# Kernel tuning notes

Measured on AMD Instinct MI355X. Metric: run time of the kernel, lower is better.

The kernel has to match this reference:

```python
import jax, jax.numpy as jnp
import numpy as np

N_NODES = 100000
N_EDGES = 500000
STALK_DIM = 16
N_TYPES = 8


def setup_inputs() -> dict:
    key = jax.random.key(0)
    k1, k2, k3, k4, k5 = jax.random.split(key, 5)
    entity_reps = jax.random.normal(k1, (STALK_DIM, N_NODES), dtype=jnp.float32)
    restriction_maps = jax.random.normal(k2, (N_TYPES, N_TYPES, STALK_DIM, STALK_DIM), dtype=jnp.float32) / STALK_DIM
    src = jax.random.randint(k3, (N_EDGES,), 0, N_NODES, dtype=jnp.int64) if jax.config.jax_enable_x64 else jax.random.randint(k3, (N_EDGES,), 0, N_NODES, dtype=jnp.int32)
    dst = jax.random.randint(k4, (N_EDGES,), 0, N_NODES, dtype=src.dtype)
    edge_index = jnp.stack([src, dst], axis=0)  # [2, E]
    entity_types = jax.random.randint(k5, (N_NODES,), 0, N_TYPES, dtype=src.dtype)
    return {"entity_reps": entity_reps, "restriction_maps": restriction_maps,
            "edge_index": edge_index, "entity_types": entity_types}


def reference(entity_reps, restriction_maps, edge_index, entity_types):
    d, n_nodes = entity_reps.shape
    n_edges = edge_index.shape[1]
    src, dst = edge_index[0], edge_index[1]

    # _get_degs: in-degree (over col) ^ -1/2, inf -> 0
    deg = jax.ops.segment_sum(jnp.ones((n_edges,), entity_reps.dtype), dst,
                              num_segments=n_nodes)
    inv_node_degs = jnp.where(deg > 0, deg ** -0.5, jnp.zeros_like(deg))

    # entity_reps @ diag(inv_node_degs): scale each node column
    x = entity_reps * inv_node_degs[None, :]  # [d, N]

    et_src = entity_types[src]  # [E]
    et_dst = entity_types[dst]  # [E]

    # Gather per-edge restriction maps [E,d,d], then replicate the original's
    # raw memory reshape to (d, d, E) (a reinterpretation, NOT a transpose).
    head_maps = restriction_maps[et_src, et_dst].reshape(d, d, n_edges)
    tail_maps = restriction_maps[et_dst, et_src].reshape(d, d, n_edges)

    # Batched per-edge matvec: head_embeddings[:, e] = head_maps[:, :, e] @ x[:, src[e]]
    head_emb = jnp.einsum('ije,je->ie', head_maps, x[:, src])  # [d, E]
    tail_emb = jnp.einsum('ije,je->ie', tail_maps, x[:, dst])  # [d, E]

    # scatter-add into per-node comparison vectors
    comparison_vec = (jnp.zeros((d, n_nodes), entity_reps.dtype)
                      .at[:, src].add(head_emb)
                      .at[:, dst].add(-tail_emb))

    # sum over d of ||row||^2 == total sum of squares
    return jnp.sum(comparison_vec ** 2)
```

## Files before the change

### kernel.cpp

```cpp
#include <hip/hip_runtime.h>
#include <math.h>

#define N_NODES 100000
#define N_EDGES 500000
#define NGRP    31250
#define NTBL    8000000

#define CHUNK   400
#define NOWN    250

#define OFF_ACC   0
#define OFF_GCNT  16
#define OFF_QBASE 1024
#define OFF_QCUR  2048
#define OFF_CV    4096
#define OFF_TP    6404096
#define OFF_XT    6904096
#define OFF_TBL   13304096
#define OFF_GQ    21304096
#define OFF_EMB   25304096
#define ZERO_BYTES 6404096

__device__ __forceinline__ unsigned owner_of(int n) {
    return (unsigned)(((unsigned long long)((unsigned)n >> 4) * 1374389535ull) >> 35);
}

__global__ __launch_bounds__(1024) void k_hist(
    const int* __restrict__ src, const int* __restrict__ dst,
    const int* __restrict__ et, unsigned char* __restrict__ tp,
    unsigned* __restrict__ gcnt) {
    __shared__ unsigned hist[NOWN];
    for (int i = threadIdx.x; i < NOWN; i += 1024) hist[i] = 0;
    __syncthreads();
    int base = blockIdx.x * 2048;
#pragma unroll
    for (int k = 0; k < 2; ++k) {
        int e = base + k * 1024 + (int)threadIdx.x;
        if (e < N_EDGES) {
            int s = src[e], d = dst[e];
            tp[e] = (unsigned char)(et[s] * 8 + et[d]);
            atomicAdd(&hist[owner_of(s)], 1u);
            atomicAdd(&hist[owner_of(d)], 1u);
        }
    }
    __syncthreads();
    for (int i = threadIdx.x; i < NOWN; i += 1024)
        if (hist[i]) atomicAdd(&gcnt[i], hist[i]);
}

__global__ void k_prefix(const unsigned* __restrict__ gcnt,
                         unsigned* __restrict__ qbase, unsigned* __restrict__ qcur) {
    __shared__ unsigned v[256];
    int t = threadIdx.x;
    v[t] = (t < NOWN) ? gcnt[t] : 0u;
    __syncthreads();
    unsigned my = v[t];
#pragma unroll
    for (int off = 1; off < 256; off <<= 1) {
        unsigned add = (t >= off) ? v[t - off] : 0u;
        __syncthreads();
        v[t] += add;
        __syncthreads();
    }
    if (t < NOWN) {
        unsigned excl = v[t] - my;
        qbase[t] = excl; qcur[t] = excl;
    }
    if (t == NOWN) qbase[NOWN] = v[NOWN - 1];
}

__global__ __launch_bounds__(1024) void k_place(
    const int* __restrict__ src, const int* __restrict__ dst,
    unsigned* __restrict__ qcur, unsigned* __restrict__ gq) {
    __shared__ unsigned hist[NOWN];
    __shared__ unsigned lcur[NOWN];
    for (int i = threadIdx.x; i < NOWN; i += 1024) hist[i] = 0;
    __syncthreads();
    int base = blockIdx.x * 2048;
#pragma unroll
    for (int k = 0; k < 2; ++k) {
        int e = base + k * 1024 + (int)threadIdx.x;
        if (e < N_EDGES) {
            atomicAdd(&hist[owner_of(src[e])], 1u);
            atomicAdd(&hist[owner_of(dst[e])], 1u);
        }
    }
    __syncthreads();
    for (int i = threadIdx.x; i < NOWN; i += 1024)
        lcur[i] = hist[i] ? atomicAdd(&qcur[i], hist[i]) : 0u;
    __syncthreads();
#pragma unroll
    for (int k = 0; k < 2; ++k) {
        int e = base + k * 1024 + (int)threadIdx.x;
        if (e < N_EDGES) {
            int s = src[e], d = dst[e];
            unsigned os = owner_of(s), od = owner_of(d);
            unsigned ps = atomicAdd(&lcur[os], 1u);
            gq[ps] = (unsigned)e | ((unsigned)(s - (int)os * CHUNK) << 19);
            unsigned pd = atomicAdd(&lcur[od], 1u);
            gq[pd] = (unsigned)e | ((unsigned)(d - (int)od * CHUNK) << 19) | (1u << 28);
        }
    }
}

__global__ __launch_bounds__(1024) void k_degxT(
    const unsigned* __restrict__ qbase, const unsigned* __restrict__ gq,
    const float* __restrict__ reps, float* __restrict__ xT) {
    __shared__ unsigned dh[CHUNK];
    for (int i = threadIdx.x; i < CHUNK; i += 1024) dh[i] = 0;
    __syncthreads();
    int o = blockIdx.x;
    unsigned lo = qbase[o], hi = qbase[o + 1];
    for (unsigned i = lo + threadIdx.x; i < hi; i += 1024) {
        unsigned ent = gq[i];
        if (ent >> 28) atomicAdd(&dh[(ent >> 19) & 511u], 1u);
    }
    __syncthreads();
    int nbase = o * CHUNK;
    for (int idx = threadIdx.x; idx < CHUNK; idx += 1024) {
        int n = nbase + idx;
        unsigned dg = dh[idx];
        float inv = dg ? 1.0f / sqrtf((float)dg) : 0.0f;
        float v[16];
#pragma unroll
        for (int j = 0; j < 16; ++j) v[j] = reps[j * N_NODES + n] * inv;
        float4* outp = (float4*)(xT + (size_t)n * 16);
#pragma unroll
        for (int j4 = 0; j4 < 4; ++j4)
            outp[j4] = make_float4(v[4*j4], v[4*j4+1], v[4*j4+2], v[4*j4+3]);
    }
}

__global__ __launch_bounds__(256) void k_tbl(const unsigned char* __restrict__ tp,
                                             unsigned char* __restrict__ tbl) {
    int idx = blockIdx.x * 256 + (int)threadIdx.x;
    int E4 = idx >> 8, q = idx & 255;
    int u = 2 * q + E4;
    int e2 = 1953 * q + (u >> 4);
    tbl[idx] = tp[e2];
}

__global__ __launch_bounds__(1024) void k_emb(
    const int* __restrict__ src, const int* __restrict__ dst,
    const unsigned char* __restrict__ tbl, const float* __restrict__ rmg,
    const float* __restrict__ xT, float* __restrict__ emb,
    int g0, int ng, int ECe) {
    __shared__ float rm[16384];
    for (int i = threadIdx.x; i < 16384; i += 1024) {
        float v = rmg[i];
        rm[i ^ ((i >> 8) & 31)] = v;
    }
    __syncthreads();

    const int wid = threadIdx.x >> 6, lane = threadIdx.x & 63;
    const int b = lane & 15, ig = lane >> 4;
    const int ntask = ng * 2;

    for (int task = blockIdx.x * 16 + wid; task < ntask; task += 256 * 16) {
        const int lgrp = task >> 1, role = task & 1;
        const int grp = g0 + lgrp;
        const int e = grp * 16 + b;
        const int node = role ? dst[e] : src[e];

        float xs[16];
        const float4* xp = (const float4*)(xT + (size_t)node * 16);
#pragma unroll
        for (int j4 = 0; j4 < 4; ++j4) {
            float4 v = xp[j4];
            xs[4*j4] = v.x; xs[4*j4+1] = v.y; xs[4*j4+2] = v.z; xs[4*j4+3] = v.w;
        }

        unsigned w[16];
        const uint4* tr4 = (const uint4*)(tbl + (size_t)grp * 256 + ig * 64);
#pragma unroll
        for (int ip = 0; ip < 4; ++ip) {
            uint4 u = tr4[ip];
            w[ip*4+0] = u.x; w[ip*4+1] = u.y; w[ip*4+2] = u.z; w[ip*4+3] = u.w;
        }
        if (role) {
#pragma unroll
            for (int c = 0; c < 16; ++c)
                w[c] = ((w[c] & 0x07070707u) << 3) | ((w[c] >> 3) & 0x07070707u);
        }

        unsigned vab[16];
#pragma unroll
        for (int jj = 0; jj < 16; ++jj)
            vab[jj] = ((unsigned)((2 * jj + grp) & 15) << 4) | (unsigned)b;

        float h0 = 0.f, h1 = 0.f, h2 = 0.f, h3 = 0.f;
#pragma unroll
        for (int ip = 0; ip < 4; ++ip) {
            float hacc = 0.f;
#pragma unroll
            for (int jj = 0; jj < 16; ++jj) {
                unsigned t = (w[ip*4 + (jj >> 2)] >> ((jj & 3) * 8)) & 255u;
                unsigned idx = ((t << 8) + vab[jj]) ^ (t & 31u);
                hacc += rm[idx] * xs[jj];
            }
            if (ip == 0) h0 = hacc; else if (ip == 1) h1 = hacc;
            else if (ip == 2) h2 = hacc; else h3 = hacc;
        }
        const int le = lgrp * 16 + b;
        float4* op = (float4*)(emb + ((size_t)role * ECe + le) * 16);
        op[ig] = make_float4(h0, h1, h2, h3);
    }
}

__global__ __launch_bounds__(1024) void k_acc(
    const unsigned* __restrict__ qbase, const unsigned* __restrict__ gq,
    const float* __restrict__ emb, float* __restrict__ cv,
    int elo, int cnt, int ECe) {
    __shared__ float cvs[CHUNK * 17];
    int o = blockIdx.x;
    int nbase = o * CHUNK;
    for (int idx = threadIdx.x; idx < CHUNK * 16; idx += 1024)
        cvs[(idx >> 4) * 17 + (idx & 15)] = cv[nbase * 16 + idx];
    __syncthreads();
    unsigned lo = qbase[o], hi = qbase[o + 1];
    for (unsigned it = lo + threadIdx.x; it < hi; it += 1024) {
        unsigned ent = gq[it];
        unsigned e = ent & 0x7FFFFu;
        if ((unsigned)(e - (unsigned)elo) >= (unsigned)cnt) continue;
        unsigned ln = (ent >> 19) & 511u, role = ent >> 28;
        unsigned le = e - (unsigned)elo;
        const float4* ep = (const float4*)(emb + ((size_t)role * ECe + le) * 16);
        float sgn = role ? -1.0f : 1.0f;
        float* c = cvs + ln * 17;
#pragma unroll
        for (int k4 = 0; k4 < 4; ++k4) {
            float4 v = ep[k4];
            atomicAdd(&c[k4*4+0], sgn * v.x);
            atomicAdd(&c[k4*4+1], sgn * v.y);
            atomicAdd(&c[k4*4+2], sgn * v.z);
            atomicAdd(&c[k4*4+3], sgn * v.w);
        }
    }
    __syncthreads();
    for (int idx = threadIdx.x; idx < CHUNK * 16; idx += 1024)
        cv[nbase * 16 + idx] = cvs[(idx >> 4) * 17 + (idx & 15)];
}

__global__ __launch_bounds__(256) void k_sq(const float* __restrict__ cv,
                                            double* __restrict__ acc) {
    __shared__ double red[4];
    int idx = blockIdx.x * 256 + (int)threadIdx.x;
    int stride = gridDim.x * 256;
    const int total4 = (16 * N_NODES) / 4;
    double p = 0.0;
    for (int i = idx; i < total4; i += stride) {
        float4 v = ((const float4*)cv)[i];
        p += (double)v.x * v.x + (double)v.y * v.y
           + (double)v.z * v.z + (double)v.w * v.w;
    }
#pragma unroll
    for (int off = 32; off > 0; off >>= 1) p += __shfl_down(p, off, 64);
    int w = threadIdx.x >> 6;
    if ((threadIdx.x & 63) == 0) red[w] = p;
    __syncthreads();
    if (threadIdx.x == 0)
        atomicAdd(acc, red[0] + red[1] + red[2] + red[3]);
}

__global__ void k_out(const double* __restrict__ acc, float* __restrict__ out) {
    out[0] = (float)acc[0];
}

extern "C" void kernel_launch(void* const* d_in, const int* in_sizes, int n_in,
                              void* d_out, int out_size, void* d_ws, size_t ws_size,
                              hipStream_t stream) {
    const float* reps = (const float*)d_in[0];
    const float* rmg  = (const float*)d_in[1];
    const int*   eidx = (const int*)d_in[2];
    const int*   et   = (const int*)d_in[3];
    const int* src = eidx;
    const int* dst = eidx + N_EDGES;

    char* ws = (char*)d_ws;
    double*        acc   = (double*)(ws + OFF_ACC);
    unsigned*      gcnt  = (unsigned*)(ws + OFF_GCNT);
    unsigned*      qbase = (unsigned*)(ws + OFF_QBASE);
    unsigned*      qcur  = (unsigned*)(ws + OFF_QCUR);
    float*         cv    = (float*)(ws + OFF_CV);
    unsigned char* tp    = (unsigned char*)(ws + OFF_TP);
    float*         xT    = (float*)(ws + OFF_XT);
    unsigned char* tbl   = (unsigned char*)(ws + OFF_TBL);
    unsigned*      gq    = (unsigned*)(ws + OFF_GQ);
    float*         emb   = (float*)(ws + OFF_EMB);

    size_t avail = (ws_size > (size_t)OFF_EMB) ? ws_size - (size_t)OFF_EMB : 0;
    int ECg = (int)(avail / 2048);
    if (ECg < 1) ECg = 1;
    if (ECg > NGRP) ECg = NGRP;
    const int ECe = ECg * 16;

    hipMemsetAsync(ws, 0, ZERO_BYTES, stream);

    k_hist  <<<245, 1024, 0, stream>>>(src, dst, et, tp, gcnt);
    k_tbl   <<<NTBL / 256, 256, 0, stream>>>(tp, tbl);
    k_prefix<<<1, 256, 0, stream>>>(gcnt, qbase, qcur);
    k_place <<<245, 1024, 0, stream>>>(src, dst, qcur, gq);
    k_degxT <<<NOWN, 1024, 0, stream>>>(qbase, gq, reps, xT);

    for (int g0 = 0; g0 < NGRP; g0 += ECg) {
        int ng = (NGRP - g0 < ECg) ? (NGRP - g0) : ECg;
        k_emb<<<256, 1024, 0, stream>>>(src, dst, tbl, rmg, xT, emb, g0, ng, ECe);
        k_acc<<<NOWN, 1024, 0, stream>>>(qbase, gq, emb, cv, g0 * 16, ng * 16, ECe);
    }

    k_sq <<<256, 256, 0, stream>>>(cv, acc);
    k_out<<<1, 1, 0, stream>>>(acc, (float*)d_out);
}
```

Measured before the change: 272.1 us.

## Write embeddings in owner-sorted order and fuse accumulation with squared-sum reduction

When the workspace is large enough, k_place records each edge's position in the owner-sorted queue. k_emb2 then writes embeddings directly to that slot with nontemporal stores, so k_accf reads them contiguously instead of gathering by edge id. k_accf accumulates into shared memory starting from zero and reduces the sum of squares directly, which removes the global cv buffer, its memset, the chunk loop and k_sq. This costs extra position arrays and scattered writes in the embedding kernel, and only applies when the workspace holds the full embedding buffer.

```diff
diff --git a/kernel.cpp b/kernel.cpp
--- a/kernel.cpp
+++ b/kernel.cpp
@@ -8,6 +8,8 @@
 
 #define CHUNK   400
 #define NOWN    250
+
+typedef float f32x4 __attribute__((ext_vector_type(4)));
 
 #define OFF_ACC   0
 #define OFF_GCNT  16
@@ -19,7 +21,7 @@
 #define OFF_TBL   13304096
 #define OFF_GQ    21304096
 #define OFF_EMB   25304096
-#define ZERO_BYTES 6404096
+#define EMB_BYTES 64000000ull
 
 __device__ __forceinline__ unsigned owner_of(int n) {
     return (unsigned)(((unsigned long long)((unsigned)n >> 4) * 1374389535ull) >> 35);
@@ -71,7 +73,8 @@
 
 __global__ __launch_bounds__(1024) void k_place(
     const int* __restrict__ src, const int* __restrict__ dst,
-    unsigned* __restrict__ qcur, unsigned* __restrict__ gq) {
+    unsigned* __restrict__ qcur, unsigned* __restrict__ gq,
+    unsigned* __restrict__ pos_h, unsigned* __restrict__ pos_t) {
     __shared__ unsigned hist[NOWN];
     __shared__ unsigned lcur[NOWN];
     for (int i = threadIdx.x; i < NOWN; i += 1024) hist[i] = 0;
@@ -97,8 +100,10 @@
             unsigned os = owner_of(s), od = owner_of(d);
             unsigned ps = atomicAdd(&lcur[os], 1u);
             gq[ps] = (unsigned)e | ((unsigned)(s - (int)os * CHUNK) << 19);
+            pos_h[e] = ps;
             unsigned pd = atomicAdd(&lcur[od], 1u);
             gq[pd] = (unsigned)e | ((unsigned)(d - (int)od * CHUNK) << 19) | (1u << 28);
+            pos_t[e] = pd;
         }
     }
 }
@@ -138,6 +143,117 @@
     int u = 2 * q + E4;
     int e2 = 1953 * q + (u >> 4);
     tbl[idx] = tp[e2];
+}
+
+__device__ __forceinline__ f32x4 emb_core(
+    int grp, int role, int b, int ig, int node,
+    const unsigned char* __restrict__ tbl, const float* __restrict__ rm,
+    const float* __restrict__ xT) {
+    float xs[16];
+    const float4* xp = (const float4*)(xT + (size_t)node * 16);
+#pragma unroll
+    for (int j4 = 0; j4 < 4; ++j4) {
+        float4 v = xp[j4];
+        xs[4*j4] = v.x; xs[4*j4+1] = v.y; xs[4*j4+2] = v.z; xs[4*j4+3] = v.w;
+    }
+    unsigned w[16];
+    const uint4* tr4 = (const uint4*)(tbl + (size_t)grp * 256 + ig * 64);
+#pragma unroll
+    for (int ip = 0; ip < 4; ++ip) {
+        uint4 u = tr4[ip];
+        w[ip*4+0] = u.x; w[ip*4+1] = u.y; w[ip*4+2] = u.z; w[ip*4+3] = u.w;
+    }
+    if (role) {
+#pragma unroll
+        for (int c = 0; c < 16; ++c)
+            w[c] = ((w[c] & 0x07070707u) << 3) | ((w[c] >> 3) & 0x07070707u);
+    }
+    unsigned vab[16];
+#pragma unroll
+    for (int jj = 0; jj < 16; ++jj)
+        vab[jj] = ((unsigned)((2 * jj + grp) & 15) << 4) | (unsigned)b;
+
+    f32x4 h;
+#pragma unroll
+    for (int ip = 0; ip < 4; ++ip) {
+        float hacc = 0.f;
+#pragma unroll
+        for (int jj = 0; jj < 16; ++jj) {
+            unsigned t = (w[ip*4 + (jj >> 2)] >> ((jj & 3) * 8)) & 255u;
+            unsigned idx = ((t << 8) + vab[jj]) ^ (t & 31u);
+            hacc += rm[idx] * xs[jj];
+        }
+        h[ip] = hacc;
+    }
+    return h;
+}
+
+__global__ __launch_bounds__(1024) void k_emb2(
+    const int* __restrict__ src, const int* __restrict__ dst,
+    const unsigned char* __restrict__ tbl, const float* __restrict__ rmg,
+    const float* __restrict__ xT, const unsigned* __restrict__ pos_h,
+    const unsigned* __restrict__ pos_t, float* __restrict__ emb2) {
+    __shared__ float rm[16384];
+    for (int i = threadIdx.x; i < 16384; i += 1024) {
+        float v = rmg[i];
+        rm[i ^ ((i >> 8) & 31)] = v;
+    }
+    __syncthreads();
+    const int wid = threadIdx.x >> 6, lane = threadIdx.x & 63;
+    const int b = lane & 15, ig = lane >> 4;
+    const int ntask = NGRP * 2;
+    for (int task = blockIdx.x * 16 + wid; task < ntask; task += 256 * 16) {
+        const int grp = task >> 1, role = task & 1;
+        const int e = grp * 16 + b;
+        const int node = role ? dst[e] : src[e];
+        f32x4 h = emb_core(grp, role, b, ig, node, tbl, rm, xT);
+        const unsigned pos = role ? pos_t[e] : pos_h[e];
+        f32x4* op = (f32x4*)(emb2 + (size_t)pos * 16);
+        __builtin_nontemporal_store(h, op + ig);
+    }
+}
+
+__global__ __launch_bounds__(1024) void k_accf(
+    const unsigned* __restrict__ qbase, const unsigned* __restrict__ gq,
+    const float* __restrict__ emb2, double* __restrict__ acc) {
+    __shared__ float cvs[CHUNK * 17];
+    __shared__ double red[16];
+    for (int i = threadIdx.x; i < CHUNK * 17; i += 1024) cvs[i] = 0.0f;
+    __syncthreads();
+    int o = blockIdx.x;
+    unsigned lo = qbase[o], hi = qbase[o + 1];
+    for (unsigned it = lo + threadIdx.x; it < hi; it += 1024) {
+        unsigned ent = gq[it];
+        unsigned ln = (ent >> 19) & 511u, role = ent >> 28;
+        const f32x4* ep = (const f32x4*)(emb2 + (size_t)it * 16);
+        float sgn = role ? -1.0f : 1.0f;
+        float* c = cvs + ln * 17;
+#pragma unroll
+        for (int k4 = 0; k4 < 4; ++k4) {
+            f32x4 v = __builtin_nontemporal_load(ep + k4);
+            atomicAdd(&c[k4*4+0], sgn * v[0]);
+            atomicAdd(&c[k4*4+1], sgn * v[1]);
+            atomicAdd(&c[k4*4+2], sgn * v[2]);
+            atomicAdd(&c[k4*4+3], sgn * v[3]);
+        }
+    }
+    __syncthreads();
+    double p = 0.0;
+    for (int idx = threadIdx.x; idx < CHUNK * 16; idx += 1024) {
+        float v = cvs[(idx >> 4) * 17 + (idx & 15)];
+        p += (double)v * v;
+    }
+#pragma unroll
+    for (int off = 32; off > 0; off >>= 1) p += __shfl_down(p, off, 64);
+    int wv = threadIdx.x >> 6;
+    if ((threadIdx.x & 63) == 0) red[wv] = p;
+    __syncthreads();
+    if (threadIdx.x == 0) {
+        double t2 = 0.0;
+#pragma unroll
+        for (int i = 0; i < 16; ++i) t2 += red[i];
+        atomicAdd(acc, t2);
+    }
 }
 
 __global__ __launch_bounds__(1024) void k_emb(
@@ -151,59 +267,18 @@
         rm[i ^ ((i >> 8) & 31)] = v;
     }
     __syncthreads();
-
     const int wid = threadIdx.x >> 6, lane = threadIdx.x & 63;
     const int b = lane & 15, ig = lane >> 4;
     const int ntask = ng * 2;
-
     for (int task = blockIdx.x * 16 + wid; task < ntask; task += 256 * 16) {
         const int lgrp = task >> 1, role = task & 1;
         const int grp = g0 + lgrp;
         const int e = grp * 16 + b;
         const int node = role ? dst[e] : src[e];
-
-        float xs[16];
-        const float4* xp = (const float4*)(xT + (size_t)node * 16);
-#pragma unroll
-        for (int j4 = 0; j4 < 4; ++j4) {
-            float4 v = xp[j4];
-            xs[4*j4] = v.x; xs[4*j4+1] = v.y; xs[4*j4+2] = v.z; xs[4*j4+3] = v.w;
-        }
-
-        unsigned w[16];
-        const uint4* tr4 = (const uint4*)(tbl + (size_t)grp * 256 + ig * 64);
-#pragma unroll
-        for (int ip = 0; ip < 4; ++ip) {
-            uint4 u = tr4[ip];
-            w[ip*4+0] = u.x; w[ip*4+1] = u.y; w[ip*4+2] = u.z; w[ip*4+3] = u.w;
-        }
-        if (role) {
-#pragma unroll
-            for (int c = 0; c < 16; ++c)
-                w[c] = ((w[c] & 0x07070707u) << 3) | ((w[c] >> 3) & 0x07070707u);
-        }
-
-        unsigned vab[16];
-#pragma unroll
-        for (int jj = 0; jj < 16; ++jj)
-            vab[jj] = ((unsigned)((2 * jj + grp) & 15) << 4) | (unsigned)b;
-
-        float h0 = 0.f, h1 = 0.f, h2 = 0.f, h3 = 0.f;
-#pragma unroll
-        for (int ip = 0; ip < 4; ++ip) {
-            float hacc = 0.f;
-#pragma unroll
-            for (int jj = 0; jj < 16; ++jj) {
-                unsigned t = (w[ip*4 + (jj >> 2)] >> ((jj & 3) * 8)) & 255u;
-                unsigned idx = ((t << 8) + vab[jj]) ^ (t & 31u);
-                hacc += rm[idx] * xs[jj];
-            }
-            if (ip == 0) h0 = hacc; else if (ip == 1) h1 = hacc;
-            else if (ip == 2) h2 = hacc; else h3 = hacc;
-        }
+        f32x4 h = emb_core(grp, role, b, ig, node, tbl, rm, xT);
         const int le = lgrp * 16 + b;
-        float4* op = (float4*)(emb + ((size_t)role * ECe + le) * 16);
-        op[ig] = make_float4(h0, h1, h2, h3);
+        f32x4* op = (f32x4*)(emb + ((size_t)role * ECe + le) * 16);
+        op[ig] = h;
     }
 }
 
@@ -288,26 +363,33 @@
     unsigned*      gq    = (unsigned*)(ws + OFF_GQ);
     float*         emb   = (float*)(ws + OFF_EMB);
 
-    size_t avail = (ws_size > (size_t)OFF_EMB) ? ws_size - (size_t)OFF_EMB : 0;
-    int ECg = (int)(avail / 2048);
-    if (ECg < 1) ECg = 1;
-    if (ECg > NGRP) ECg = NGRP;
-    const int ECe = ECg * 16;
-
-    hipMemsetAsync(ws, 0, ZERO_BYTES, stream);
+    const bool single = ws_size >= (size_t)OFF_EMB + EMB_BYTES;
+    unsigned* pos_h = single ? (unsigned*)(ws + OFF_CV) : (unsigned*)(ws + OFF_EMB);
+    unsigned* pos_t = pos_h + N_EDGES;
+
+    (void)hipMemsetAsync(ws, 0, single ? 1024 : 6404096, stream);
 
     k_hist  <<<245, 1024, 0, stream>>>(src, dst, et, tp, gcnt);
     k_tbl   <<<NTBL / 256, 256, 0, stream>>>(tp, tbl);
     k_prefix<<<1, 256, 0, stream>>>(gcnt, qbase, qcur);
-    k_place <<<245, 1024, 0, stream>>>(src, dst, qcur, gq);
+    k_place <<<245, 1024, 0, stream>>>(src, dst, qcur, gq, pos_h, pos_t);
     k_degxT <<<NOWN, 1024, 0, stream>>>(qbase, gq, reps, xT);
 
-    for (int g0 = 0; g0 < NGRP; g0 += ECg) {
-        int ng = (NGRP - g0 < ECg) ? (NGRP - g0) : ECg;
-        k_emb<<<256, 1024, 0, stream>>>(src, dst, tbl, rmg, xT, emb, g0, ng, ECe);
-        k_acc<<<NOWN, 1024, 0, stream>>>(qbase, gq, emb, cv, g0 * 16, ng * 16, ECe);
-    }
-
-    k_sq <<<256, 256, 0, stream>>>(cv, acc);
+    if (single) {
+        k_emb2<<<256, 1024, 0, stream>>>(src, dst, tbl, rmg, xT, pos_h, pos_t, emb);
+        k_accf<<<NOWN, 1024, 0, stream>>>(qbase, gq, emb, acc);
+    } else {
+        size_t avail = (ws_size > (size_t)OFF_EMB) ? ws_size - (size_t)OFF_EMB : 2048;
+        int ECg = (int)(avail / 2048);
+        if (ECg < 1) ECg = 1;
+        if (ECg > NGRP) ECg = NGRP;
+        const int ECe = ECg * 16;
+        for (int g0 = 0; g0 < NGRP; g0 += ECg) {
+            int ng = (NGRP - g0 < ECg) ? (NGRP - g0) : ECg;
+            k_emb<<<256, 1024, 0, stream>>>(src, dst, tbl, rmg, xT, emb, g0, ng, ECe);
+            k_acc<<<NOWN, 1024, 0, stream>>>(qbase, gq, emb, cv, g0 * 16, ng * 16, ECe);
+        }
+        k_sq<<<256, 256, 0, stream>>>(cv, acc);
+    }
     k_out<<<1, 1, 0, stream>>>(acc, (float*)d_out);
 }
```

Measured after the change: 276.8 us. No clear change (+1.7%).
